# Kernel tuning notes

Measured on AMD Instinct MI355X. Metric: run time of the kernel, lower is better.

## Reference

```python
import jax, jax.numpy as jnp
import numpy as np

BLOCK_LEN = 64


def segsum(x):
    """x: (..., T) -> (..., T, T) with segsum[i,j] = sum_{k=j+1..i} x[k] (lower-tri incl diag), -inf above."""
    T = x.shape[-1]
    xc = jnp.cumsum(x, axis=-1)
    seg = xc[..., :, None] - xc[..., None, :]
    mask = jnp.tril(jnp.ones((T, T), dtype=bool))
    return jnp.where(mask, seg, -jnp.inf)


def setup_inputs() -> dict:
    key = jax.random.key(0)
    kx, ka, kb, kc = jax.random.split(key, 4)
    b, s, h, p, n = 4, 4096, 32, 64, 64
    X = jax.random.normal(kx, (b, s, h), dtype=jnp.float32)  # placeholder to keep split order stable
    X = jax.random.normal(kx, (b, s, h, p), dtype=jnp.float32)
    # A must be negative for a stable SSM decay (exp of cumulative sums stays bounded)
    A = -jax.random.uniform(ka, (b, s, h), dtype=jnp.float32, minval=0.0, maxval=1.0)
    B = jax.random.normal(kb, (b, s, h, n), dtype=jnp.float32)
    C = jax.random.normal(kc, (b, s, h, n), dtype=jnp.float32)
    return {"X": X, "A": A, "B": B, "C": C}


def reference(X, A, B, C):
    blk = BLOCK_LEN
    b, s, h, p = X.shape
    n = B.shape[-1]
    c = s // blk
    # chunk: b (c l) ... -> b c l ...
    Xc = X.reshape(b, c, blk, h, p)
    Bc = B.reshape(b, c, blk, h, n)
    Cc = C.reshape(b, c, blk, h, n)
    Ac = A.reshape(b, c, blk, h).transpose(0, 3, 1, 2)  # b h c l
    A_cumsum = jnp.cumsum(Ac, axis=-1)                  # b h c l

    # 1. intra-chunk (diagonal block) output
    L = jnp.exp(segsum(Ac))                             # b h c l s
    Y_diag = jnp.einsum("bclhn,bcshn,bhcls,bcshp->bclhp", Cc, Bc, L, Xc)

    # 2. intra-chunk states (chunk-final state assuming zero initial state)
    decay_states = jnp.exp(A_cumsum[..., -1:] - A_cumsum)
    states = jnp.einsum("bclhn,bhcl,bclhp->bchpn", Bc, decay_states, Xc)

    # 3. inter-chunk recurrence over chunk boundaries
    init = jnp.zeros_like(states[:, :1])
    states = jnp.concatenate([init, states], axis=1)    # b (c+1) h p n
    A_last = jnp.pad(A_cumsum[..., -1], ((0, 0), (0, 0), (1, 0)))  # b h (c+1)
    decay_chunk = jnp.exp(segsum(A_last))               # b h (c+1) (c+1)
    new_states = jnp.einsum("bhzc,bchpn->bzhpn", decay_chunk, states)
    states_in = new_states[:, :-1]                      # state entering each chunk

    # 4. state -> output
    state_decay_out = jnp.exp(A_cumsum)
    Y_off = jnp.einsum("bclhn,bchpn,bhcl->bclhp", Cc, states_in, state_decay_out)

    Y = (Y_diag + Y_off).reshape(b, s, h, p)
    return Y
```

## Files before the change

kernel.cpp:

```cpp
#include <hip/hip_runtime.h>

namespace {

typedef __attribute__((ext_vector_type(8))) short short8;
typedef __attribute__((ext_vector_type(16))) float f32x16;

constexpr int Hh = 32, Ssq = 4096, NCH = 64;
constexpr int GR = 2048;
constexpr int ST = 72;

__device__ inline unsigned short f2bf(float f) {
  unsigned u = __float_as_uint(f);
  u += 0x7FFFu + ((u >> 16) & 1u);
  return (unsigned short)(u >> 16);
}
__device__ inline float bf2f(unsigned short s) {
  return __uint_as_float(((unsigned)s) << 16);
}

__device__ inline short8 frag128(const unsigned short* base, int row, int ks, int lhi) {
  return *(const short8*)(base + row * ST + ks * 16 + lhi * 8);
}

__global__ __launch_bounds__(256, 8)
void k1a_chunkstate(const float* __restrict__ X0, const float* __restrict__ A0,
                    const float* __restrict__ B0, unsigned short* __restrict__ S16) {
  __shared__ __align__(16) unsigned short BTs[64 * ST];
  __shared__ __align__(16) unsigned short XTs[64 * ST];
  __shared__ float ielb[64];
  __shared__ float eab;

  const int tid = threadIdx.x;
  const int hi = blockIdx.x & 31, ci = (blockIdx.x >> 5) & 63, bi = blockIdx.x >> 11;
  if (ci == 63) return;

  const float* Xg = X0 + (((size_t)bi * Ssq + ci * 64) * Hh + hi) * 64;
  const float* Bg = B0 + (((size_t)bi * Ssq + ci * 64) * Hh + hi) * 64;
  const float* Ag = A0 + ((size_t)bi * Ssq + ci * 64) * Hh + hi;
  unsigned short* sp = S16 + ((size_t)(bi * Hh + hi) * NCH + ci) * 4096;

  const int w = tid >> 6, lane = tid & 63;
  const int l31 = lane & 31, lhi = lane >> 5;

  if (tid < 64) {
    float a = Ag[(size_t)tid * Hh];
#pragma unroll
    for (int off = 1; off < 64; off <<= 1) {
      float v = __shfl_up(a, off);
      if (tid >= off) a += v;
    }
    ielb[tid] = __expf(-a);
    if (tid == 63) eab = __expf(a);
  }
  __syncthreads();

  {
    const int r = tid >> 2, cb = (tid & 3) * 4;
    const float iel = ielb[r];
    const float* bp = Bg + (size_t)r * GR;
    const float* xp = Xg + (size_t)r * GR;
#pragma unroll
    for (int j = 0; j < 4; ++j) {
      const int c = cb + 16 * j;
      float4 bv = *(const float4*)(bp + c);
      BTs[(c + 0) * ST + r] = f2bf(bv.x * iel);
      BTs[(c + 1) * ST + r] = f2bf(bv.y * iel);
      BTs[(c + 2) * ST + r] = f2bf(bv.z * iel);
      BTs[(c + 3) * ST + r] = f2bf(bv.w * iel);
      float4 xv = *(const float4*)(xp + c);
      XTs[(c + 0) * ST + r] = f2bf(xv.x);
      XTs[(c + 1) * ST + r] = f2bf(xv.y);
      XTs[(c + 2) * ST + r] = f2bf(xv.z);
      XTs[(c + 3) * ST + r] = f2bf(xv.w);
    }
  }
  __syncthreads();

  const int tp = w >> 1, tn = w & 1;
  f32x16 acc = {};
#pragma unroll
  for (int ks = 0; ks < 4; ++ks)
    acc = __builtin_amdgcn_mfma_f32_32x32x16_bf16(
        frag128(XTs, 32 * tp + l31, ks, lhi),
        frag128(BTs, 32 * tn + l31, ks, lhi),
        acc, 0, 0, 0);
  const float ea = eab;
#pragma unroll
  for (int i = 0; i < 16; ++i) {
    const int p = 32 * tp + (i & 3) + 8 * (i >> 2) + 4 * lhi;
    sp[p * 64 + 32 * tn + l31] = f2bf(acc[i] * ea);
  }
}

__global__ __launch_bounds__(256)
void k1b_scan(const float* __restrict__ A0, unsigned short* __restrict__ S16) {
  __shared__ float part[256];
  __shared__ float eat[64];

  const int tid = threadIdx.x;
  const int sl8 = blockIdx.x & 7, hi = (blockIdx.x >> 3) & 31, bi = blockIdx.x >> 8;
  const float* Ag = A0 + (size_t)bi * Ssq * Hh + hi;

  {
    const int c = tid >> 2, q = tid & 3;
    float s = 0.f;
#pragma unroll
    for (int k = 0; k < 16; ++k) s += Ag[(size_t)(c * 64 + q * 16 + k) * Hh];
    part[tid] = s;
  }
  __syncthreads();
  if (tid < 64)
    eat[tid] = __expf(part[tid * 4] + part[tid * 4 + 1] + part[tid * 4 + 2] + part[tid * 4 + 3]);
  __syncthreads();

  unsigned short* base =
      S16 + (size_t)(bi * Hh + hi) * NCH * 4096 + sl8 * 512 + tid * 2;
  float s0 = 0.f, s1 = 0.f;

  auto L = [&](int c) -> unsigned {
    return (c < 63) ? *(const unsigned*)(base + (size_t)c * 4096) : 0u;
  };
  auto step = [&](int c, unsigned v) {
    const float ea = eat[c];
    s0 = s0 * ea + bf2f((unsigned short)(v & 0xffffu));
    s1 = s1 * ea + bf2f((unsigned short)(v >> 16));
    *(unsigned*)(base + (size_t)(c + 1) * 4096) =
        (unsigned)f2bf(s0) | ((unsigned)f2bf(s1) << 16);
  };

  unsigned q0 = L(0), q1 = L(1), q2 = L(2), q3 = L(3);
  for (int c = 0; c < 60; c += 4) {
    step(c + 0, q0); q0 = L(c + 4);
    step(c + 1, q1); q1 = L(c + 5);
    step(c + 2, q2); q2 = L(c + 6);
    step(c + 3, q3); q3 = L(c + 7);
  }
  step(60, q0); step(61, q1); step(62, q2);
}

__global__ __launch_bounds__(256, 5)
void k2_y(const float* __restrict__ X0, const float* __restrict__ A0,
          const float* __restrict__ B0, const float* __restrict__ C0,
          const unsigned short* __restrict__ S16, float* __restrict__ Y0) {
  __shared__ __align__(16) unsigned short Cs[64 * ST];
  __shared__ __align__(16) unsigned short Bsh[64 * ST];
  __shared__ __align__(16) unsigned short XT[64 * ST];
  __shared__ float elb[64], ielb2[64];

  const int tid = threadIdx.x;
  const int hi = blockIdx.x & 31, ci = (blockIdx.x >> 5) & 63, bi = blockIdx.x >> 11;

  const float* Xg = X0 + (((size_t)bi * Ssq + ci * 64) * Hh + hi) * 64;
  const float* Bg = B0 + (((size_t)bi * Ssq + ci * 64) * Hh + hi) * 64;
  const float* Cg = C0 + (((size_t)bi * Ssq + ci * 64) * Hh + hi) * 64;
  const float* Ag = A0 + ((size_t)bi * Ssq + ci * 64) * Hh + hi;
  const unsigned short* Sg = S16 + ((size_t)(bi * Hh + hi) * NCH + ci) * 4096;
  float* Yg = Y0 + (((size_t)bi * Ssq + ci * 64) * Hh + hi) * 64;

  const int w = tid >> 6, lane = tid & 63;
  const int l31 = lane & 31, lhi = lane >> 5;

  if (tid < 64) {
    float a = Ag[(size_t)tid * Hh];
#pragma unroll
    for (int off = 1; off < 64; off <<= 1) {
      float v = __shfl_up(a, off);
      if (tid >= off) a += v;
    }
    elb[tid] = __expf(a);
    ielb2[tid] = __expf(-a);
  }
  __syncthreads();

  {
    const int r = tid >> 2, cb = (tid & 3) * 4;
    const float iel = ielb2[r];
    const float* bp = Bg + (size_t)r * GR;
    const float* cp = Cg + (size_t)r * GR;
    const float* xp = Xg + (size_t)r * GR;
#pragma unroll
    for (int j = 0; j < 4; ++j) {
      const int c = cb + 16 * j;
      float4 bv = *(const float4*)(bp + c);
      float4 cv = *(const float4*)(cp + c);
      unsigned short bb[4] = {f2bf(bv.x * iel), f2bf(bv.y * iel),
                              f2bf(bv.z * iel), f2bf(bv.w * iel)};
      unsigned short cc[4] = {f2bf(cv.x), f2bf(cv.y), f2bf(cv.z), f2bf(cv.w)};
      *(uint2*)&Bsh[r * ST + c] = *(const uint2*)bb;
      *(uint2*)&Cs[r * ST + c] = *(const uint2*)cc;
      float4 xv = *(const float4*)(xp + c);
      XT[(c + 0) * ST + r] = f2bf(xv.x);
      XT[(c + 1) * ST + r] = f2bf(xv.y);
      XT[(c + 2) * ST + r] = f2bf(xv.z);
      XT[(c + 3) * ST + r] = f2bf(xv.w);
    }
  }
  __syncthreads();

  const int ati = (w == 0) ? 0 : 1;
  const int atj = (w == 2) ? 1 : 0;
  f32x16 ga = {};
  if (w < 3) {
#pragma unroll
    for (int ks = 0; ks < 4; ++ks)
      ga = __builtin_amdgcn_mfma_f32_32x32x16_bf16(
          frag128(Cs, 32 * ati + l31, ks, lhi),
          frag128(Bsh, 32 * atj + l31, ks, lhi),
          ga, 0, 0, 0);
  }
  __syncthreads();

  if (w < 3) {
    const int gcol = 32 * atj + l31;
#pragma unroll
    for (int i = 0; i < 16; ++i) {
      const int grow = 32 * ati + (i & 3) + 8 * (i >> 2) + 4 * lhi;
      float gv = (gcol <= grow) ? ga[i] * elb[grow] : 0.f;
      Bsh[grow * ST + gcol] = f2bf(gv);
    }
  } else {
    const short8 z8 = {};
    *(short8*)&Bsh[l31 * ST + 32 + lhi * 16] = z8;
    *(short8*)&Bsh[l31 * ST + 40 + lhi * 16] = z8;
  }
  __syncthreads();

  {
    const int ti = w >> 1, tj = w & 1;
    short8 sf[4];
    if (ci != 0) {
      const unsigned short* srow = Sg + (32 * tj + l31) * 64;
#pragma unroll
      for (int ks = 0; ks < 4; ++ks)
        sf[ks] = *(const short8*)(srow + ks * 16 + lhi * 8);
    }
    f32x16 aD = {}, aO = {};
#pragma unroll
    for (int ks = 0; ks < 4; ++ks)
      aD = __builtin_amdgcn_mfma_f32_32x32x16_bf16(
          frag128(Bsh, 32 * ti + l31, ks, lhi),
          frag128(XT, 32 * tj + l31, ks, lhi),
          aD, 0, 0, 0);
    if (ci != 0) {
#pragma unroll
      for (int ks = 0; ks < 4; ++ks)
        aO = __builtin_amdgcn_mfma_f32_32x32x16_bf16(
            frag128(Cs, 32 * ti + l31, ks, lhi),
            sf[ks],
            aO, 0, 0, 0);
    }
#pragma unroll
    for (int i = 0; i < 16; ++i) {
      const int row = 32 * ti + (i & 3) + 8 * (i >> 2) + 4 * lhi;
      Yg[(size_t)row * GR + 32 * tj + l31] = aD[i] + elb[row] * aO[i];
    }
  }
}

}

extern "C" void kernel_launch(void* const* d_in, const int* in_sizes, int n_in,
                              void* d_out, int out_size, void* d_ws, size_t ws_size,
                              hipStream_t stream) {
  const float* X = (const float*)d_in[0];
  const float* A = (const float*)d_in[1];
  const float* B = (const float*)d_in[2];
  const float* C = (const float*)d_in[3];
  float* Y = (float*)d_out;
  unsigned short* S16 = (unsigned short*)d_ws;
  (void)in_sizes; (void)n_in; (void)out_size; (void)ws_size;
  k1a_chunkstate<<<dim3(8192), dim3(256), 0, stream>>>(X, A, B, S16);
  k1b_scan<<<dim3(1024), dim3(256), 0, stream>>>(A, S16);
  k2_y<<<dim3(8192), dim3(256), 0, stream>>>(X, A, B, C, S16, Y);
}
```

Before: 240.8 us.

## Load MFMA fragments for C and B straight from global, prefetch X and states

In k2_y, the C and B tiles no longer go through shared memory. Each wave loads its MFMA fragments straight from global and converts them to bf16 in registers. The decay scaling exp(-A) moves from B into the G epilogue, and G is now computed by all four waves instead of three, which removes a sync and the zero-fill path. The X and state loads are issued before the cumsum prefix so global latency overlaps with it, and both kernels get occupancy hints of 6. The cost is redundant global loads of C (read twice per wave) and more register pressure.

```diff
diff --git a/kernel.cpp b/kernel.cpp
--- a/kernel.cpp
+++ b/kernel.cpp
@@ -18,11 +18,26 @@
   return __uint_as_float(((unsigned)s) << 16);
 }
 
+__device__ inline short8 pack8(float4 a, float4 b) {
+  short8 o;
+  o[0] = (short)f2bf(a.x); o[1] = (short)f2bf(a.y);
+  o[2] = (short)f2bf(a.z); o[3] = (short)f2bf(a.w);
+  o[4] = (short)f2bf(b.x); o[5] = (short)f2bf(b.y);
+  o[6] = (short)f2bf(b.z); o[7] = (short)f2bf(b.w);
+  return o;
+}
+
 __device__ inline short8 frag128(const unsigned short* base, int row, int ks, int lhi) {
   return *(const short8*)(base + row * ST + ks * 16 + lhi * 8);
 }
-
-__global__ __launch_bounds__(256, 8)
+__device__ inline short8 gfrag(const float* rowp, int ks, int lhi) {
+  const int off = ks * 16 + lhi * 8;
+  float4 a = *(const float4*)(rowp + off);
+  float4 b = *(const float4*)(rowp + off + 4);
+  return pack8(a, b);
+}
+
+__global__ __launch_bounds__(256, 6)
 void k1a_chunkstate(const float* __restrict__ X0, const float* __restrict__ A0,
                     const float* __restrict__ B0, unsigned short* __restrict__ S16) {
   __shared__ __align__(16) unsigned short BTs[64 * ST];
@@ -42,6 +57,15 @@
   const int w = tid >> 6, lane = tid & 63;
   const int l31 = lane & 31, lhi = lane >> 5;
 
+  const int r = tid >> 2, cb = (tid & 3) * 4;
+  float4 bv[4], xv[4];
+#pragma unroll
+  for (int j = 0; j < 4; ++j) {
+    const int c = cb + 16 * j;
+    bv[j] = *(const float4*)(Bg + (size_t)r * GR + c);
+    xv[j] = *(const float4*)(Xg + (size_t)r * GR + c);
+  }
+
   if (tid < 64) {
     float a = Ag[(size_t)tid * Hh];
 #pragma unroll
@@ -55,23 +79,18 @@
   __syncthreads();
 
   {
-    const int r = tid >> 2, cb = (tid & 3) * 4;
     const float iel = ielb[r];
-    const float* bp = Bg + (size_t)r * GR;
-    const float* xp = Xg + (size_t)r * GR;
 #pragma unroll
     for (int j = 0; j < 4; ++j) {
       const int c = cb + 16 * j;
-      float4 bv = *(const float4*)(bp + c);
-      BTs[(c + 0) * ST + r] = f2bf(bv.x * iel);
-      BTs[(c + 1) * ST + r] = f2bf(bv.y * iel);
-      BTs[(c + 2) * ST + r] = f2bf(bv.z * iel);
-      BTs[(c + 3) * ST + r] = f2bf(bv.w * iel);
-      float4 xv = *(const float4*)(xp + c);
-      XTs[(c + 0) * ST + r] = f2bf(xv.x);
-      XTs[(c + 1) * ST + r] = f2bf(xv.y);
-      XTs[(c + 2) * ST + r] = f2bf(xv.z);
-      XTs[(c + 3) * ST + r] = f2bf(xv.w);
+      BTs[(c + 0) * ST + r] = f2bf(bv[j].x * iel);
+      BTs[(c + 1) * ST + r] = f2bf(bv[j].y * iel);
+      BTs[(c + 2) * ST + r] = f2bf(bv[j].z * iel);
+      BTs[(c + 3) * ST + r] = f2bf(bv[j].w * iel);
+      XTs[(c + 0) * ST + r] = f2bf(xv[j].x);
+      XTs[(c + 1) * ST + r] = f2bf(xv[j].y);
+      XTs[(c + 2) * ST + r] = f2bf(xv[j].z);
+      XTs[(c + 3) * ST + r] = f2bf(xv[j].w);
     }
   }
   __syncthreads();
@@ -82,8 +101,7 @@
   for (int ks = 0; ks < 4; ++ks)
     acc = __builtin_amdgcn_mfma_f32_32x32x16_bf16(
         frag128(XTs, 32 * tp + l31, ks, lhi),
-        frag128(BTs, 32 * tn + l31, ks, lhi),
-        acc, 0, 0, 0);
+        frag128(BTs, 32 * tn + l31, ks, lhi), acc, 0, 0, 0);
   const float ea = eab;
 #pragma unroll
   for (int i = 0; i < 16; ++i) {
@@ -138,14 +156,13 @@
   step(60, q0); step(61, q1); step(62, q2);
 }
 
-__global__ __launch_bounds__(256, 5)
+__global__ __launch_bounds__(256, 6)
 void k2_y(const float* __restrict__ X0, const float* __restrict__ A0,
           const float* __restrict__ B0, const float* __restrict__ C0,
           const unsigned short* __restrict__ S16, float* __restrict__ Y0) {
-  __shared__ __align__(16) unsigned short Cs[64 * ST];
-  __shared__ __align__(16) unsigned short Bsh[64 * ST];
+  __shared__ __align__(16) unsigned short Gs[64 * ST];
   __shared__ __align__(16) unsigned short XT[64 * ST];
-  __shared__ float elb[64], ielb2[64];
+  __shared__ float elb[64], ielb[64];
 
   const int tid = threadIdx.x;
   const int hi = blockIdx.x & 31, ci = (blockIdx.x >> 5) & 63, bi = blockIdx.x >> 11;
@@ -159,6 +176,21 @@
 
   const int w = tid >> 6, lane = tid & 63;
   const int l31 = lane & 31, lhi = lane >> 5;
+  const int ti = w >> 1, tj = w & 1;
+
+  const int r = tid >> 2, cb = (tid & 3) * 4;
+  float4 xv[4];
+#pragma unroll
+  for (int j = 0; j < 4; ++j)
+    xv[j] = *(const float4*)(Xg + (size_t)r * GR + cb + 16 * j);
+
+  short8 sf[4] = {};
+  if (ci != 0) {
+    const unsigned short* srow = Sg + (32 * tj + l31) * 64;
+#pragma unroll
+    for (int ks = 0; ks < 4; ++ks)
+      sf[ks] = *(const short8*)(srow + ks * 16 + lhi * 8);
+  }
 
   if (tid < 64) {
     float a = Ag[(size_t)tid * Hh];
@@ -168,86 +200,62 @@
       if (tid >= off) a += v;
     }
     elb[tid] = __expf(a);
-    ielb2[tid] = __expf(-a);
-  }
-  __syncthreads();
-
-  {
-    const int r = tid >> 2, cb = (tid & 3) * 4;
-    const float iel = ielb2[r];
-    const float* bp = Bg + (size_t)r * GR;
-    const float* cp = Cg + (size_t)r * GR;
-    const float* xp = Xg + (size_t)r * GR;
+    ielb[tid] = __expf(-a);
+  }
+
+  {
 #pragma unroll
     for (int j = 0; j < 4; ++j) {
       const int c = cb + 16 * j;
-      float4 bv = *(const float4*)(bp + c);
-      float4 cv = *(const float4*)(cp + c);
-      unsigned short bb[4] = {f2bf(bv.x * iel), f2bf(bv.y * iel),
-                              f2bf(bv.z * iel), f2bf(bv.w * iel)};
-      unsigned short cc[4] = {f2bf(cv.x), f2bf(cv.y), f2bf(cv.z), f2bf(cv.w)};
-      *(uint2*)&Bsh[r * ST + c] = *(const uint2*)bb;
-      *(uint2*)&Cs[r * ST + c] = *(const uint2*)cc;
-      float4 xv = *(const float4*)(xp + c);
-      XT[(c + 0) * ST + r] = f2bf(xv.x);
-      XT[(c + 1) * ST + r] = f2bf(xv.y);
-      XT[(c + 2) * ST + r] = f2bf(xv.z);
-      XT[(c + 3) * ST + r] = f2bf(xv.w);
-    }
-  }
-  __syncthreads();
-
-  const int ati = (w == 0) ? 0 : 1;
-  const int atj = (w == 2) ? 1 : 0;
-  f32x16 ga = {};
-  if (w < 3) {
+      XT[(c + 0) * ST + r] = f2bf(xv[j].x);
+      XT[(c + 1) * ST + r] = f2bf(xv[j].y);
+      XT[(c + 2) * ST + r] = f2bf(xv[j].z);
+      XT[(c + 3) * ST + r] = f2bf(xv[j].w);
+    }
+  }
+  __syncthreads();
+
+  {
+    const float* crow = Cg + (size_t)(32 * ti + l31) * GR;
+    const float* brow = Bg + (size_t)(32 * tj + l31) * GR;
+    short8 af[4], bf[4];
+#pragma unroll
+    for (int ks = 0; ks < 4; ++ks) {
+      af[ks] = gfrag(crow, ks, lhi);
+      bf[ks] = gfrag(brow, ks, lhi);
+    }
+    f32x16 ga = {};
 #pragma unroll
     for (int ks = 0; ks < 4; ++ks)
-      ga = __builtin_amdgcn_mfma_f32_32x32x16_bf16(
-          frag128(Cs, 32 * ati + l31, ks, lhi),
-          frag128(Bsh, 32 * atj + l31, ks, lhi),
-          ga, 0, 0, 0);
-  }
-  __syncthreads();
-
-  if (w < 3) {
-    const int gcol = 32 * atj + l31;
+      ga = __builtin_amdgcn_mfma_f32_32x32x16_bf16(af[ks], bf[ks], ga, 0, 0, 0);
+
+    const int gcol = 32 * tj + l31;
+    const float ielc = ielb[gcol];
 #pragma unroll
     for (int i = 0; i < 16; ++i) {
-      const int grow = 32 * ati + (i & 3) + 8 * (i >> 2) + 4 * lhi;
-      float gv = (gcol <= grow) ? ga[i] * elb[grow] : 0.f;
-      Bsh[grow * ST + gcol] = f2bf(gv);
-    }
-  } else {
-    const short8 z8 = {};
-    *(short8*)&Bsh[l31 * ST + 32 + lhi * 16] = z8;
-    *(short8*)&Bsh[l31 * ST + 40 + lhi * 16] = z8;
-  }
-  __syncthreads();
-
-  {
-    const int ti = w >> 1, tj = w & 1;
-    short8 sf[4];
-    if (ci != 0) {
-      const unsigned short* srow = Sg + (32 * tj + l31) * 64;
-#pragma unroll
-      for (int ks = 0; ks < 4; ++ks)
-        sf[ks] = *(const short8*)(srow + ks * 16 + lhi * 8);
-    }
+      const int grow = 32 * ti + (i & 3) + 8 * (i >> 2) + 4 * lhi;
+      float gv = (gcol <= grow) ? ga[i] * (elb[grow] * ielc) : 0.f;
+      Gs[grow * ST + gcol] = f2bf(gv);
+    }
+  }
+  __syncthreads();
+
+  {
+    const float* crow = Cg + (size_t)(32 * ti + l31) * GR;
+    short8 cf[4];
+#pragma unroll
+    for (int ks = 0; ks < 4; ++ks) cf[ks] = gfrag(crow, ks, lhi);
+
     f32x16 aD = {}, aO = {};
 #pragma unroll
     for (int ks = 0; ks < 4; ++ks)
       aD = __builtin_amdgcn_mfma_f32_32x32x16_bf16(
-          frag128(Bsh, 32 * ti + l31, ks, lhi),
-          frag128(XT, 32 * tj + l31, ks, lhi),
-          aD, 0, 0, 0);
+          frag128(Gs, 32 * ti + l31, ks, lhi),
+          frag128(XT, 32 * tj + l31, ks, lhi), aD, 0, 0, 0);
     if (ci != 0) {
 #pragma unroll
       for (int ks = 0; ks < 4; ++ks)
-        aO = __builtin_amdgcn_mfma_f32_32x32x16_bf16(
-            frag128(Cs, 32 * ti + l31, ks, lhi),
-            sf[ks],
-            aO, 0, 0, 0);
+        aO = __builtin_amdgcn_mfma_f32_32x32x16_bf16(cf[ks], sf[ks], aO, 0, 0, 0);
     }
 #pragma unroll
     for (int i = 0; i < 16; ++i) {
```

Result: slower. 297.4 us (+23.5%).
